# Kernel optimization log

Measured on AMD Instinct MI355X. Metric: run time of the kernel, lower is better.

The kernel has to match this reference:

```python
import jax, jax.numpy as jnp
import numpy as np

B, S, D, H, F = 2, 2048, 1024, 16, 4096
HD = D // H
EPS = 1e-5
NEG = -1e9


def _layernorm(x, g, b):
    mu = jnp.mean(x, axis=-1, keepdims=True)
    var = jnp.mean((x - mu) ** 2, axis=-1, keepdims=True)
    return (x - mu) * jax.lax.rsqrt(var + EPS) * g + b


def _attention(x, wq, wk, wv, wo, bo):
    b, s, d = x.shape
    q = (x @ wq).reshape(b, s, H, HD).transpose(0, 2, 1, 3)  # [b,h,s,hd]
    k = (x @ wk).reshape(b, s, H, HD).transpose(0, 2, 1, 3)
    v = (x @ wv).reshape(b, s, H, HD).transpose(0, 2, 1, 3)
    scores = jnp.einsum('bhqd,bhkd->bhqk', q, k) / (HD ** 0.5)
    # Faithful to source bug: masked_fill(mask == 0, -1e9) where mask = triu(diag=1)
    # -> positions with k <= q (lower triangle incl. diagonal) are filled with -1e9.
    lower = jnp.tril(jnp.ones((s, s), dtype=bool))
    scores = jnp.where(lower, NEG, scores)
    w = jax.nn.softmax(scores, axis=-1)
    o = jnp.einsum('bhqk,bhkd->bhqd', w, v)
    o = o.transpose(0, 2, 1, 3).reshape(b, s, d)
    return o @ wo + bo


def _ffn(x, w1, b1, w2, b2):
    return jax.nn.gelu(x @ w1 + b1, approximate=False) @ w2 + b2


def setup_inputs() -> dict:
    key = jax.random.key(0)
    ks = jax.random.split(key, 10)
    s = 0.02
    return {
        'x': jax.random.normal(ks[0], (B, S, D), jnp.float32),
        'wq': jax.random.normal(ks[1], (D, D), jnp.float32) * s,
        'wk': jax.random.normal(ks[2], (D, D), jnp.float32) * s,
        'wv': jax.random.normal(ks[3], (D, D), jnp.float32) * s,
        'wo': jax.random.normal(ks[4], (D, D), jnp.float32) * s,
        'bo': jnp.zeros((D,), jnp.float32),
        'ln1_g': jnp.ones((D,), jnp.float32),
        'ln1_b': jnp.zeros((D,), jnp.float32),
        'ln2_g': jnp.ones((D,), jnp.float32),
        'ln2_b': jnp.zeros((D,), jnp.float32),
        'w1': jax.random.normal(ks[5], (D, F), jnp.float32) * s,
        'b1': jnp.zeros((F,), jnp.float32),
        'w2': jax.random.normal(ks[6], (F, D), jnp.float32) * s,
        'b2': jnp.zeros((D,), jnp.float32),
    }


def reference(x, wq, wk, wv, wo, bo, ln1_g, ln1_b, ln2_g, ln2_b, w1, b1, w2, b2):
    shortcut = x
    h = _layernorm(x, ln1_g, ln1_b)
    h = _attention(h, wq, wk, wv, wo, bo)  # dropout = identity (eval)
    h = h + shortcut
    shortcut = h
    h2 = _layernorm(h, ln2_g, ln2_b)
    h2 = _attention(h2, wq, wk, wv, wo, bo)  # same attn module reused, per source
    h2 = _ffn(h2, w1, b1, w2, b2)
    return h2 + shortcut
```

## Files before the change

### kernel.cpp

```cpp
#include <hip/hip_runtime.h>
#include <hip/hip_bf16.h>
#include <math.h>

#define Bz 2
#define Sz 2048
#define Dz 1024
#define Hz 16
#define HDz 64
#define Fz 4096
#define ROWS (Bz*Sz)
#define EPSf 1e-5f
#define NEGf -1e9f

typedef __attribute__((ext_vector_type(8))) short short8;
typedef __attribute__((ext_vector_type(4))) float floatx4;

__device__ __forceinline__ unsigned short f2bf(float f){
  __hip_bfloat16 h = __float2bfloat16(f);
  return *(unsigned short*)&h;
}
__device__ __forceinline__ float bf2f(unsigned short u){
  union { unsigned x; float f; } a; a.x = ((unsigned)u) << 16; return a.f;
}

__device__ __forceinline__ float fast_gelu(float x){
  float t  = fabsf(x) * 0.70710678118654752f;
  float kk = __builtin_amdgcn_rcpf(1.0f + 0.3275911f * t);
  float poly = ((((1.061405429f*kk - 1.453152027f)*kk + 1.421413741f)*kk
                 - 0.284496736f)*kk + 0.254829592f)*kk;
  float er = 1.0f - poly * __expf(-t*t);
  er = copysignf(er, x);
  return 0.5f * x * (1.0f + er);
}

__device__ __forceinline__ void gload16(const void* g, void* l){
  __builtin_amdgcn_global_load_lds(
      (const __attribute__((address_space(1))) unsigned int*)g,
      (__attribute__((address_space(3))) unsigned int*)l, 16, 0, 0);
}

__device__ __forceinline__ void bar(){
  asm volatile("" ::: "memory");
  __builtin_amdgcn_s_barrier();
  asm volatile("" ::: "memory");
}
#define WAITV6 asm volatile("s_waitcnt vmcnt(6)" ::: "memory")
#define WAITV0 asm volatile("s_waitcnt vmcnt(0)" ::: "memory")
#define WL0    asm volatile("s_waitcnt lgkmcnt(0)" ::: "memory")

__device__ __forceinline__ void xcd_remap(int& bmblk, int& bnblk){
  int gx = gridDim.x, gy = gridDim.y;
  int id = blockIdx.y * gx + blockIdx.x;
  int xcd = id & 7, local = id >> 3;
  bnblk = local % gx;
  bmblk = xcd * (gy >> 3) + local / gx;
}

__global__ __launch_bounds__(256)
void transpose_cast(const float* __restrict__ W, unsigned short* __restrict__ Wt,
                    int K, int N)
{
  __shared__ unsigned short Ts[32][33];
  int n0 = blockIdx.x*32, k0 = blockIdx.y*32;
  int r = threadIdx.x >> 3, c0 = (threadIdx.x & 7) * 4;
  float4 w4 = *(const float4*)(W + (size_t)(k0+r)*N + n0 + c0);
  Ts[r][c0+0] = f2bf(w4.x); Ts[r][c0+1] = f2bf(w4.y);
  Ts[r][c0+2] = f2bf(w4.z); Ts[r][c0+3] = f2bf(w4.w);
  __syncthreads();
  unsigned v0 = Ts[c0+0][r], v1 = Ts[c0+1][r], v2 = Ts[c0+2][r], v3 = Ts[c0+3][r];
  uint2 p; p.x = v0 | (v1<<16); p.y = v2 | (v3<<16);
  *(uint2*)(Wt + (size_t)(n0+r)*K + k0 + c0) = p;
}

__global__ __launch_bounds__(256)
void ln_kernel(const float* __restrict__ in, const float* __restrict__ gam,
               const float* __restrict__ bet, unsigned short* __restrict__ out)
{
  int row = blockIdx.x, t = threadIdx.x;
  size_t base = (size_t)row * Dz;
  int c0 = t * 4;
  float4 x4 = *(const float4*)(in + base + c0);
  float v[4] = {x4.x, x4.y, x4.z, x4.w};
  float s = v[0]+v[1]+v[2]+v[3];
  #pragma unroll
  for (int off=32; off>0; off>>=1) s += __shfl_down(s, off, 64);
  __shared__ float ws[4];
  int lane = t & 63, wid = t >> 6;
  if (lane == 0) ws[wid] = s;
  __syncthreads();
  float mu = (ws[0]+ws[1]+ws[2]+ws[3]) * (1.0f/Dz);
  __syncthreads();
  float d0=v[0]-mu, d1=v[1]-mu, d2=v[2]-mu, d3=v[3]-mu;
  float s2 = d0*d0+d1*d1+d2*d2+d3*d3;
  #pragma unroll
  for (int off=32; off>0; off>>=1) s2 += __shfl_down(s2, off, 64);
  if (lane == 0) ws[wid] = s2;
  __syncthreads();
  float var = (ws[0]+ws[1]+ws[2]+ws[3]) * (1.0f/Dz);
  float rstd = rsqrtf(var + EPSf);
  float4 g4 = *(const float4*)(gam + c0);
  float4 b4 = *(const float4*)(bet + c0);
  unsigned r0 = f2bf((v[0]-mu)*rstd*g4.x + b4.x);
  unsigned r1 = f2bf((v[1]-mu)*rstd*g4.y + b4.y);
  unsigned r2 = f2bf((v[2]-mu)*rstd*g4.z + b4.z);
  unsigned r3 = f2bf((v[3]-mu)*rstd*g4.w + b4.w);
  uint2 p; p.x = r0 | (r1<<16); p.y = r2 | (r3<<16);
  *(uint2*)(out + base + c0) = p;
}

#define STG_A(buf, half, k0) { \
  _Pragma("unroll") for (int c_=0;c_<2;c_++){ \
    int sg_ = c_*8 + wave; \
    int row0_ = ((sg_>>3)<<7) + ((sg_&7)<<3) + ((half)<<6); \
    gload16(pA[half][c_] + (k0), &As[buf][row0_*64]); } }

#define STG_B(buf, jh, k0) { \
  _Pragma("unroll") for (int c_=0;c_<2;c_++){ \
    int sg_ = c_*8 + wave; int rho0_ = sg_<<3; \
    gload16(pB[jh][c_] + (k0), &Bs[buf][jh][rho0_*64]); } }

#define READ_A4(dst, buf, ihalf) { \
  _Pragma("unroll") for (int ii_=0; ii_<4; ++ii_){ \
    int row_ = wm*128 + ((ihalf)*4+ii_)*16 + l15; \
    _Pragma("unroll") for (int ks_=0; ks_<2; ++ks_){ \
      int slot_ = (ks_*4+quad) ^ (l15&7); \
      dst[ii_][ks_] = *(const short8*)&As[buf][row_*64 + slot_*8]; } } }

#define READ_B2(dst, buf, jh) { \
  _Pragma("unroll") for (int jl_=0; jl_<2; ++jl_){ \
    int rho_ = wn*32 + jl_*16 + l15; \
    _Pragma("unroll") for (int ks_=0; ks_<2; ++ks_){ \
      int slot_ = (ks_*4+quad) ^ (l15&7); \
      dst[jl_][ks_] = *(const short8*)&Bs[buf][jh][rho_*64 + slot_*8]; } } }

#define MFMA_PH(IH, JH, AF, BF) { \
  __builtin_amdgcn_s_setprio(1); \
  _Pragma("unroll") for (int ii_=0; ii_<4; ++ii_){ \
    _Pragma("unroll") for (int jl_=0; jl_<2; ++jl_){ \
      floatx4 c_ = acc[(IH)*4+ii_][(JH)*2+jl_]; \
      c_ = __builtin_amdgcn_mfma_f32_16x16x32_bf16(AF[ii_][0], BF[jl_][0], c_, 0,0,0); \
      c_ = __builtin_amdgcn_mfma_f32_16x16x32_bf16(AF[ii_][1], BF[jl_][1], c_, 0,0,0); \
      acc[(IH)*4+ii_][(JH)*2+jl_] = c_; } } \
  __builtin_amdgcn_s_setprio(0); }

__global__ __launch_bounds__(512, 2)
void gemm256(const unsigned short* __restrict__ A,
             const unsigned short* __restrict__ Bt,
             const float* __restrict__ bias, const float* __restrict__ res,
             float* __restrict__ outf, unsigned short* __restrict__ outb,
             int M, int N, int K, int lda, int ldb, int act, int qkvmode)
{
  __shared__ unsigned short As[2][256*64];
  __shared__ unsigned short Bs[2][2][128*64];

  int t = threadIdx.x;
  int wave = t >> 6, lane = t & 63;
  int l15 = lane & 15, quad = lane >> 4;
  int wm = wave >> 2, wn = wave & 3;

  int nN = gridDim.x, nM = gridDim.y;
  int id = blockIdx.y * nN + blockIdx.x;
  int xcd = id & 7, local = id >> 3;
  int bnblk = local % nN;
  int bmblk = xcd * (nM >> 3) + local / nN;
  int bm = bmblk * 256, bn = bnblk * 256;

  if (gridDim.z > 1){
    A    += (size_t)blockIdx.z * K;
    Bt   += (size_t)blockIdx.z * K;
    outf += (size_t)blockIdx.z * ((size_t)M * N);
  }

  int lrow = lane >> 3;
  int lcol = ((lane & 7) ^ (lane >> 3)) * 8;

  const unsigned short* pA[2][2];
  const unsigned short* pB[2][2];
  #pragma unroll
  for (int half=0; half<2; half++)
    #pragma unroll
    for (int c=0;c<2;c++){
      int sg = c*8 + wave;
      int row0 = ((sg>>3)<<7) + ((sg&7)<<3) + (half<<6);
      pA[half][c] = A + (size_t)(bm + row0 + lrow)*lda + lcol;
    }
  #pragma unroll
  for (int jh=0; jh<2; jh++)
    #pragma unroll
    for (int c=0;c<2;c++){
      int sg = c*8 + wave;
      int rho0 = sg<<3;
      int gn = ((rho0>>5)<<6) + (jh<<5) + (rho0&31);
      pB[jh][c] = Bt + (size_t)(bn + gn + lrow)*ldb + lcol;
    }

  floatx4 acc[8][4];
  #pragma unroll
  for (int i=0;i<8;i++)
    #pragma unroll
    for (int j=0;j<4;j++) acc[i][j] = (floatx4){0.f,0.f,0.f,0.f};

  STG_A(0, 0, 0);  STG_A(0, 1, 0);
  STG_B(0, 0, 0);  STG_B(0, 1, 0);
  STG_A(1, 0, 64); STG_A(1, 1, 64);
  STG_B(1, 0, 64);
  WAITV6;
  bar();

  int NKT = K >> 6;
  int nIter = NKT >> 1;
  for (int it = 0; it < nIter; ++it){
    bool more = (it + 1 < nIter);
    int k0B  = (2*it+1) << 6;
    int k0A2 = (2*it+2) << 6;
    int k0B2 = (2*it+3) << 6;
    short8 aLo[4][2], aHi[4][2], bcur[2][2];

    READ_A4(aLo, 0, 0);
    READ_B2(bcur, 0, 0);
    STG_B(1, 1, k0B);
    bar(); WL0;
    MFMA_PH(0, 0, aLo, bcur);
    bar();

    READ_A4(aHi, 0, 1);
    READ_B2(bcur, 0, 0);
    if (more) STG_A(0, 0, k0A2);
    bar(); WL0;
    MFMA_PH(1, 0, aHi, bcur);
    bar();

    READ_B2(bcur, 0, 1);
    if (more) STG_A(0, 1, k0A2);
    bar(); WL0;
    MFMA_PH(0, 1, aLo, bcur);
    bar();

    if (more) { STG_B(0, 0, k0A2); WAITV6; }
    else      { WAITV0; }
    bar();
    MFMA_PH(1, 1, aHi, bcur);
    bar();

    READ_A4(aLo, 1, 0);
    READ_B2(bcur, 1, 0);
    if (more) STG_B(0, 1, k0A2);
    bar(); WL0;
    MFMA_PH(0, 0, aLo, bcur);
    bar();

    READ_A4(aHi, 1, 1);
    READ_B2(bcur, 1, 0);
    if (more) STG_A(1, 0, k0B2);
    bar(); WL0;
    MFMA_PH(1, 0, aHi, bcur);
    bar();

    READ_B2(bcur, 1, 1);
    if (more) STG_A(1, 1, k0B2);
    bar(); WL0;
    MFMA_PH(0, 1, aLo, bcur);
    bar();

    if (more) { STG_B(1, 0, k0B2); WAITV6; }
    bar();
    MFMA_PH(1, 1, aHi, bcur);
    bar();
  }

  float bj[4];
  #pragma unroll
  for (int j=0;j<4;j++) bj[j] = bias ? bias[bn + wn*64 + j*16 + l15] : 0.f;

  size_t selbase = 0; int ncol = N; int bnl = bn;
  if (qkvmode){ selbase = (size_t)(bn >> 10) * ((size_t)M * 1024); ncol = 1024; bnl = bn & 1023; }

  #pragma unroll
  for (int i=0;i<8;i++){
    int row0 = bm + wm*128 + i*16 + quad*4;
    #pragma unroll
    for (int r=0;r<4;r++){
      size_t rowoff = selbase + (size_t)(row0 + r) * ncol;
      #pragma unroll
      for (int j=0;j<4;j++){
        float v = acc[i][j][r] + bj[j];
        if (act) v = fast_gelu(v);
        size_t off = rowoff + bnl + wn*64 + j*16 + l15;
        if (res) v += res[off];
        if (outf) outf[off] = v;
        else      outb[off] = f2bf(v);
      }
    }
  }
}

__global__ __launch_bounds__(256)
void gemm_n64(const unsigned short* __restrict__ A,
              const unsigned short* __restrict__ Bt,
              const float* __restrict__ bias, const float* __restrict__ res,
              float* __restrict__ outf, unsigned short* __restrict__ outb,
              int M, int N, int K)
{
  __shared__ unsigned short As[2][128*64];
  __shared__ unsigned short Bs[2][64*64];
  int t = threadIdx.x;
  int bmblk, bnblk; xcd_remap(bmblk, bnblk);
  int bm = bmblk * 128, bn = bnblk * 64;
  int wave = t >> 6, lane = t & 63;
  int l15 = lane & 15, quad = lane >> 4;
  int arow = lane >> 3;
  int acbg = ((lane & 7) ^ arow) * 8;
  const unsigned short* gA = A  + (size_t)(bm + wave*32 + arow)*K + acbg;
  const unsigned short* gB = Bt + (size_t)(bn + wave*16 + arow)*K + acbg;

  floatx4 acc[2][4];
  #pragma unroll
  for (int i=0;i<2;i++)
    #pragma unroll
    for (int j=0;j<4;j++) acc[i][j] = (floatx4){0.f,0.f,0.f,0.f};

  int swr = (l15 & 7);

  {
    unsigned short* lA = &As[0][wave*32*64];
    unsigned short* lB = &Bs[0][wave*16*64];
    gload16(gA,                 lA);
    gload16(gA + (size_t)8*K,   lA + 8*64);
    gload16(gA + (size_t)16*K,  lA + 16*64);
    gload16(gA + (size_t)24*K,  lA + 24*64);
    gload16(gB,                 lB);
    gload16(gB + (size_t)8*K,   lB + 8*64);
  }

  int nIter = K >> 6;
  for (int it = 0; it < nIter; ++it) {
    __syncthreads();
    int cur = it & 1;
    if (it + 1 < nIter) {
      int k1 = (it+1) << 6;
      unsigned short* lA = &As[cur^1][wave*32*64];
      unsigned short* lB = &Bs[cur^1][wave*16*64];
      gload16(gA + k1,                 lA);
      gload16(gA + k1 + (size_t)8*K,   lA + 8*64);
      gload16(gA + k1 + (size_t)16*K,  lA + 16*64);
      gload16(gA + k1 + (size_t)24*K,  lA + 24*64);
      gload16(gB + k1,                 lB);
      gload16(gB + k1 + (size_t)8*K,   lB + 8*64);
    }
    const unsigned short* Ac = As[cur];
    const unsigned short* Bc = Bs[cur];
    #pragma unroll
    for (int ks=0; ks<2; ++ks){
      short8 af[2], bf[4];
      #pragma unroll
      for (int i=0;i<2;i++)
        af[i] = *(const short8*)&Ac[(wave*32 + i*16 + l15)*64 + ((ks*4 + quad) ^ swr)*8];
      #pragma unroll
      for (int j=0;j<4;j++)
        bf[j] = *(const short8*)&Bc[(j*16 + l15)*64 + ((ks*4 + quad) ^ swr)*8];
      #pragma unroll
      for (int i=0;i<2;i++)
        #pragma unroll
        for (int j=0;j<4;j++)
          acc[i][j] = __builtin_amdgcn_mfma_f32_16x16x32_bf16(af[i], bf[j], acc[i][j], 0, 0, 0);
    }
  }

  float bj[4];
  #pragma unroll
  for (int j=0;j<4;j++) bj[j] = bias ? bias[bn + j*16 + l15] : 0.f;

  #pragma unroll
  for (int i=0;i<2;i++){
    int row0 = bm + wave*32 + i*16 + quad*4;
    #pragma unroll
    for (int r=0;r<4;r++){
      size_t rowoff = (size_t)(row0 + r) * N;
      #pragma unroll
      for (int j=0;j<4;j++){
        float v = acc[i][j][r] + bj[j];
        size_t off = rowoff + bn + j*16 + l15;
        if (res) v += res[off];
        if (outf) outf[off] = v;
        else      outb[off] = f2bf(v);
      }
    }
  }
}

__global__ __launch_bounds__(256)
void reduce4(const float* __restrict__ part, const float* __restrict__ bias,
             const float* __restrict__ res, float* __restrict__ out)
{
  const size_t NN = (size_t)ROWS * Dz;
  size_t i = ((size_t)blockIdx.x * 256 + threadIdx.x) * 4;
  float4 a = *(const float4*)(part + i);
  float4 b = *(const float4*)(part + NN + i);
  float4 c = *(const float4*)(part + 2*NN + i);
  float4 d = *(const float4*)(part + 3*NN + i);
  float4 r = *(const float4*)(res + i);
  int col = threadIdx.x * 4;
  float4 g = *(const float4*)(bias + col);
  float4 o;
  o.x = a.x+b.x+c.x+d.x + g.x + r.x;
  o.y = a.y+b.y+c.y+d.y + g.y + r.y;
  o.z = a.z+b.z+c.z+d.z + g.z + r.z;
  o.w = a.w+b.w+c.w+d.w + g.w + r.w;
  *(float4*)(out + i) = o;
}

__global__ __launch_bounds__(256)
void vmean_kernel(const unsigned short* __restrict__ v, float* __restrict__ vm)
{
  int h = blockIdx.x, b = blockIdx.y;
  int t = threadIdx.x, d = t & 63, seg = t >> 6;
  float s = 0.f;
  for (int i=0;i<512;i++){
    int srow = seg*512 + i;
    s += bf2f(v[((size_t)(b*Sz + srow))*Dz + h*HDz + d]);
  }
  __shared__ float red[4][64];
  red[seg][d] = s;
  __syncthreads();
  if (seg == 0){
    float tot = red[0][d]+red[1][d]+red[2][d]+red[3][d];
    vm[(b*Hz + h)*HDz + d] = tot * (1.0f/2048.0f);
  }
}

__global__ __launch_bounds__(256)
void attn_mfma(const unsigned short* __restrict__ Qg,
               const unsigned short* __restrict__ Kg,
               const unsigned short* __restrict__ Vg,
               const float* __restrict__ vmean,
               unsigned short* __restrict__ Og)
{
  __shared__ unsigned short Ks[128][72];
  __shared__ unsigned short Vts[64][136];
  __shared__ unsigned short Ps[128][72];

  int t = threadIdx.x;
  int wave = t >> 6, lane = t & 63;
  int l15 = lane & 15, quad = lane >> 4;
  int b = blockIdx.z, h = blockIdx.y;
  int qt = b ? (15 - (int)blockIdx.x) : (int)blockIdx.x;

  {
    int r = t >> 1, c = (t & 1) * 32;
    const unsigned short* qp = Qg + ((size_t)(b*Sz + qt*128 + r))*Dz + h*HDz + c;
    uint4 q0 = *(const uint4*)(qp);
    uint4 q1 = *(const uint4*)(qp + 8);
    uint4 q2 = *(const uint4*)(qp + 16);
    uint4 q3 = *(const uint4*)(qp + 24);
    *(uint4*)&Ps[r][c]      = q0;
    *(uint4*)&Ps[r][c + 8]  = q1;
    *(uint4*)&Ps[r][c + 16] = q2;
    *(uint4*)&Ps[r][c + 24] = q3;
  }
  __syncthreads();
  short8 aq[2][2];
  #pragma unroll
  for (int i=0;i<2;i++)
    #pragma unroll
    for (int ks=0;ks<2;ks++)
      aq[i][ks] = *(const short8*)&Ps[wave*32 + i*16 + l15][ks*32 + quad*8];

  floatx4 acc_o[2][4];
  #pragma unroll
  for (int i=0;i<2;i++)
    #pragma unroll
    for (int j=0;j<4;j++) acc_o[i][j] = (floatx4){0.f,0.f,0.f,0.f};
  float lacc[2][4];
  #pragma unroll
  for (int i=0;i<2;i++)
    #pragma unroll
    for (int r=0;r<4;r++) lacc[i][r] = 0.f;

  int sr = t >> 2, sc = (t & 3) * 16;

  uint4 pk0,pk1,pk2,pk3,pv0,pv1,pv2,pv3;
  {
    size_t off0 = ((size_t)(b*Sz + qt*128 + sr))*Dz + h*HDz + sc;
    size_t off1 = off0 + (size_t)64*Dz;
    pk0 = *(const uint4*)(Kg + off0); pk1 = *(const uint4*)(Kg + off0 + 8);
    pk2 = *(const uint4*)(Kg + off1); pk3 = *(const uint4*)(Kg + off1 + 8);
    pv0 = *(const uint4*)(Vg + off0); pv1 = *(const uint4*)(Vg + off0 + 8);
    pv2 = *(const uint4*)(Vg + off1); pv3 = *(const uint4*)(Vg + off1 + 8);
  }

  for (int jt2 = qt; jt2 < Sz/128; ++jt2) {
    __syncthreads();
    {
      *(uint4*)&Ks[sr][sc]        = pk0; *(uint4*)&Ks[sr][sc + 8]      = pk1;
      *(uint4*)&Ks[64 + sr][sc]   = pk2; *(uint4*)&Ks[64 + sr][sc + 8] = pk3;
      unsigned short e[16];
      e[0]=pv0.x&0xffff; e[1]=pv0.x>>16; e[2]=pv0.y&0xffff; e[3]=pv0.y>>16;
      e[4]=pv0.z&0xffff; e[5]=pv0.z>>16; e[6]=pv0.w&0xffff; e[7]=pv0.w>>16;
      e[8]=pv1.x&0xffff; e[9]=pv1.x>>16; e[10]=pv1.y&0xffff; e[11]=pv1.y>>16;
      e[12]=pv1.z&0xffff; e[13]=pv1.z>>16; e[14]=pv1.w&0xffff; e[15]=pv1.w>>16;
      #pragma unroll
      for (int j=0;j<16;j++) Vts[sc + j][sr] = e[j];
      e[0]=pv2.x&0xffff; e[1]=pv2.x>>16; e[2]=pv2.y&0xffff; e[3]=pv2.y>>16;
      e[4]=pv2.z&0xffff; e[5]=pv2.z>>16; e[6]=pv2.w&0xffff; e[7]=pv2.w>>16;
      e[8]=pv3.x&0xffff; e[9]=pv3.x>>16; e[10]=pv3.y&0xffff; e[11]=pv3.y>>16;
      e[12]=pv3.z&0xffff; e[13]=pv3.z>>16; e[14]=pv3.w&0xffff; e[15]=pv3.w>>16;
      #pragma unroll
      for (int j=0;j<16;j++) Vts[sc + j][64 + sr] = e[j];
    }
    __syncthreads();

    if (jt2 + 1 < Sz/128) {
      size_t off0 = ((size_t)(b*Sz + (jt2+1)*128 + sr))*Dz + h*HDz + sc;
      size_t off1 = off0 + (size_t)64*Dz;
      pk0 = *(const uint4*)(Kg + off0); pk1 = *(const uint4*)(Kg + off0 + 8);
      pk2 = *(const uint4*)(Kg + off1); pk3 = *(const uint4*)(Kg + off1 + 8);
      pv0 = *(const uint4*)(Vg + off0); pv1 = *(const uint4*)(Vg + off0 + 8);
      pv2 = *(const uint4*)(Vg + off1); pv3 = *(const uint4*)(Vg + off1 + 8);
    }

    #pragma unroll
    for (int hh=0; hh<2; ++hh){
      floatx4 acc_s[2][4];
      #pragma unroll
      for (int i=0;i<2;i++)
        #pragma unroll
        for (int j=0;j<4;j++) acc_s[i][j] = (floatx4){0.f,0.f,0.f,0.f};
      #pragma unroll
      for (int ks=0;ks<2;ks++){
        short8 bk[4];
        #pragma unroll
        for (int j=0;j<4;j++) bk[j] = *(const short8*)&Ks[hh*64 + j*16 + l15][ks*32 + quad*8];
        #pragma unroll
        for (int i=0;i<2;i++)
          #pragma unroll
          for (int j=0;j<4;j++)
            acc_s[i][j] = __builtin_amdgcn_mfma_f32_16x16x32_bf16(aq[i][ks], bk[j], acc_s[i][j], 0, 0, 0);
      }
      #pragma unroll
      for (int i=0;i<2;i++){
        #pragma unroll
        for (int j=0;j<4;j++){
          int kj = jt2*128 + hh*64 + j*16 + l15;
          #pragma unroll
          for (int r=0;r<4;r++){
            int qrow = qt*128 + wave*32 + i*16 + quad*4 + r;
            float s = acc_s[i][j][r] * 0.125f;
            if (kj <= qrow) s = NEGf;
            float p = __expf(fminf(s, 80.f));
            lacc[i][r] += p;
            Ps[wave*32 + i*16 + quad*4 + r][j*16 + l15] = f2bf(p);
          }
        }
      }
      #pragma unroll
      for (int ks=0;ks<2;ks++){
        short8 ap[2], bv[4];
        #pragma unroll
        for (int i=0;i<2;i++) ap[i] = *(const short8*)&Ps[wave*32 + i*16 + l15][ks*32 + quad*8];
        #pragma unroll
        for (int j=0;j<4;j++) bv[j] = *(const short8*)&Vts[j*16 + l15][hh*64 + ks*32 + quad*8];
        #pragma unroll
        for (int i=0;i<2;i++)
          #pragma unroll
          for (int j=0;j<4;j++)
            acc_o[i][j] = __builtin_amdgcn_mfma_f32_16x16x32_bf16(ap[i], bv[j], acc_o[i][j], 0, 0, 0);
      }
    }
  }

  #pragma unroll
  for (int i=0;i<2;i++){
    #pragma unroll
    for (int r=0;r<4;r++){
      float l = lacc[i][r];
      l += __shfl_xor(l, 1, 64);
      l += __shfl_xor(l, 2, 64);
      l += __shfl_xor(l, 4, 64);
      l += __shfl_xor(l, 8, 64);
      int qrow = qt*128 + wave*32 + i*16 + quad*4 + r;
      float inv = 1.0f / l;
      size_t rowoff = ((size_t)(b*Sz + qrow))*Dz + h*HDz;
      #pragma unroll
      for (int j=0;j<4;j++){
        float ov = acc_o[i][j][r] * inv;
        if (qrow == Sz-1) ov = vmean[(b*Hz + h)*HDz + j*16 + l15];
        Og[rowoff + j*16 + l15] = f2bf(ov);
      }
    }
  }
}

extern "C" void kernel_launch(void* const* d_in, const int* in_sizes, int n_in,
                              void* d_out, int out_size, void* d_ws, size_t ws_size,
                              hipStream_t stream)
{
  const float* x    = (const float*)d_in[0];
  const float* wq   = (const float*)d_in[1];
  const float* wk   = (const float*)d_in[2];
  const float* wv   = (const float*)d_in[3];
  const float* wo   = (const float*)d_in[4];
  const float* bo   = (const float*)d_in[5];
  const float* ln1g = (const float*)d_in[6];
  const float* ln1b = (const float*)d_in[7];
  const float* ln2g = (const float*)d_in[8];
  const float* ln2b = (const float*)d_in[9];
  const float* w1   = (const float*)d_in[10];
  const float* b1   = (const float*)d_in[11];
  const float* w2   = (const float*)d_in[12];
  const float* b2   = (const float*)d_in[13];
  float* out = (float*)d_out;

  const size_t MB = 1024*1024;
  char* w = (char*)d_ws;
  float*          trunk = (float*)(w);
  unsigned short* lnb   = (unsigned short*)(w + 16*MB);
  float*          vmean = (float*)(w + 16*MB);
  unsigned short* q     = (unsigned short*)(w + 24*MB);
  unsigned short* k     = (unsigned short*)(w + 32*MB);
  unsigned short* v     = (unsigned short*)(w + 40*MB);
  unsigned short* ctx   = (unsigned short*)(w + 48*MB);
  unsigned short* wqkvT = (unsigned short*)(w + 56*MB);
  unsigned short* wqT   = wqkvT;
  unsigned short* wkT   = (unsigned short*)(w + 58*MB);
  unsigned short* wvT   = (unsigned short*)(w + 60*MB);
  unsigned short* woT   = (unsigned short*)(w + 62*MB);
  unsigned short* w1T   = (unsigned short*)(w + 64*MB);
  unsigned short* w2T   = (unsigned short*)(w + 72*MB);
  unsigned short* mid   = (unsigned short*)(w + 24*MB);
  float*          part  = (float*)(w + 80*MB);
  bool splitk = ws_size >= (size_t)144*MB;

  dim3 blk(256), blk512(512);
  transpose_cast<<<dim3(32,32),  blk, 0, stream>>>(wq, wqT, Dz, Dz);
  transpose_cast<<<dim3(32,32),  blk, 0, stream>>>(wk, wkT, Dz, Dz);
  transpose_cast<<<dim3(32,32),  blk, 0, stream>>>(wv, wvT, Dz, Dz);
  transpose_cast<<<dim3(32,32),  blk, 0, stream>>>(wo, woT, Dz, Dz);
  transpose_cast<<<dim3(128,32), blk, 0, stream>>>(w1, w1T, Dz, Fz);
  transpose_cast<<<dim3(32,128), blk, 0, stream>>>(w2, w2T, Fz, Dz);

  dim3 gln(ROWS);
  dim3 gqkv(3*Dz/256, ROWS/256);
  dim3 gf1(Fz/256,  ROWS/256);
  dim3 gn64(Dz/64,  ROWS/128);
  dim3 gattn(Sz/128, Hz, Bz);
  dim3 gvm(Hz, Bz);

  ln_kernel<<<gln, blk, 0, stream>>>(x, ln1g, ln1b, lnb);
  gemm256<<<gqkv, blk512, 0, stream>>>(lnb, wqkvT, nullptr, nullptr, nullptr, q, ROWS, 3*Dz, Dz, Dz, Dz, 0, 1);
  vmean_kernel<<<gvm, blk, 0, stream>>>(v, vmean);
  attn_mfma<<<gattn, blk, 0, stream>>>(q, k, v, vmean, ctx);
  gemm_n64<<<gn64, blk, 0, stream>>>(ctx, woT, bo, x, trunk, nullptr, ROWS, Dz, Dz);

  ln_kernel<<<gln, blk, 0, stream>>>(trunk, ln2g, ln2b, lnb);
  gemm256<<<gqkv, blk512, 0, stream>>>(lnb, wqkvT, nullptr, nullptr, nullptr, q, ROWS, 3*Dz, Dz, Dz, Dz, 0, 1);
  vmean_kernel<<<gvm, blk, 0, stream>>>(v, vmean);
  attn_mfma<<<gattn, blk, 0, stream>>>(q, k, v, vmean, ctx);
  gemm_n64<<<gn64, blk, 0, stream>>>(ctx, woT, bo, nullptr, nullptr, lnb, ROWS, Dz, Dz);
  gemm256<<<gf1, blk512, 0, stream>>>(lnb, w1T, b1, nullptr, nullptr, mid, ROWS, Fz, Dz, Dz, Dz, 1, 0);
  if (splitk) {
    gemm256<<<dim3(4,16,4), blk512, 0, stream>>>(mid, w2T, nullptr, nullptr, part, nullptr, ROWS, Dz, Fz/4, Fz, Fz, 0, 0);
    reduce4<<<dim3(4096), blk, 0, stream>>>(part, b2, trunk, out);
  } else {
    gemm_n64<<<gn64, blk, 0, stream>>>(mid, w2T, b2, trunk, out, nullptr, ROWS, Dz, Fz);
  }
}
```

Baseline: 540.1 us.

## Pre-transpose V globally and use XOR-swizzled LDS layouts for K and V in attention

Adds a bf16 transpose kernel that writes V as [b,h,d,s] into scratch space borrowed from the output buffer. The attention kernel can then load V^T tiles with vector stores instead of scattering 16 scalar LDS writes per thread. K and V^T tiles now use unpadded LDS layouts with XOR swizzling to avoid bank conflicts. The cost is an extra transpose launch and its memory traffic per attention call, plus reliance on the output buffer being free as scratch until the final kernel writes it.

```diff
diff --git a/kernel.cpp b/kernel.cpp
--- a/kernel.cpp
+++ b/kernel.cpp
@@ -70,6 +70,25 @@
   unsigned v0 = Ts[c0+0][r], v1 = Ts[c0+1][r], v2 = Ts[c0+2][r], v3 = Ts[c0+3][r];
   uint2 p; p.x = v0 | (v1<<16); p.y = v2 | (v3<<16);
   *(uint2*)(Wt + (size_t)(n0+r)*K + k0 + c0) = p;
+}
+
+__global__ __launch_bounds__(256)
+void transpose_bf(const unsigned short* __restrict__ V, unsigned short* __restrict__ VT)
+{
+  __shared__ unsigned short Ts[32][33];
+  int st = blockIdx.x*32;
+  int R0 = blockIdx.y*32;
+  int b = R0 >> 10, hd0 = R0 & 1023;
+  int r = threadIdx.x >> 3, c0 = (threadIdx.x & 7) * 4;
+  uint2 w = *(const uint2*)(V + (size_t)(b*Sz + st + r)*Dz + hd0 + c0);
+  Ts[r][c0+0] = (unsigned short)(w.x & 0xffff);
+  Ts[r][c0+1] = (unsigned short)(w.x >> 16);
+  Ts[r][c0+2] = (unsigned short)(w.y & 0xffff);
+  Ts[r][c0+3] = (unsigned short)(w.y >> 16);
+  __syncthreads();
+  unsigned v0 = Ts[c0+0][r], v1 = Ts[c0+1][r], v2 = Ts[c0+2][r], v3 = Ts[c0+3][r];
+  uint2 p; p.x = v0 | (v1<<16); p.y = v2 | (v3<<16);
+  *(uint2*)(VT + (size_t)(R0+r)*Sz + st + c0) = p;
 }
 
 __global__ __launch_bounds__(256)
@@ -431,12 +450,12 @@
 __global__ __launch_bounds__(256)
 void attn_mfma(const unsigned short* __restrict__ Qg,
                const unsigned short* __restrict__ Kg,
-               const unsigned short* __restrict__ Vg,
+               const unsigned short* __restrict__ VTg,
                const float* __restrict__ vmean,
                unsigned short* __restrict__ Og)
 {
-  __shared__ unsigned short Ks[128][72];
-  __shared__ unsigned short Vts[64][136];
+  __shared__ unsigned short Ks[128*64];
+  __shared__ unsigned short Vts[64*128];
   __shared__ unsigned short Ps[128][72];
 
   int t = threadIdx.x;
@@ -477,6 +496,9 @@
     for (int r=0;r<4;r++) lacc[i][r] = 0.f;
 
   int sr = t >> 2, sc = (t & 3) * 16;
+  int kc2 = (t & 3) * 2, ksw = sr & 7;
+  int vd = t >> 2, vc = t & 3, vsw = vd & 7;
+  const unsigned short* vrow = VTg + ((size_t)((b*Hz + h)*64 + vd))*Sz;
 
   uint4 pk0,pk1,pk2,pk3,pv0,pv1,pv2,pv3;
   {
@@ -484,28 +506,23 @@
     size_t off1 = off0 + (size_t)64*Dz;
     pk0 = *(const uint4*)(Kg + off0); pk1 = *(const uint4*)(Kg + off0 + 8);
     pk2 = *(const uint4*)(Kg + off1); pk3 = *(const uint4*)(Kg + off1 + 8);
-    pv0 = *(const uint4*)(Vg + off0); pv1 = *(const uint4*)(Vg + off0 + 8);
-    pv2 = *(const uint4*)(Vg + off1); pv3 = *(const uint4*)(Vg + off1 + 8);
+    int vo = qt*128 + vc*32;
+    pv0 = *(const uint4*)(vrow + vo);      pv1 = *(const uint4*)(vrow + vo + 8);
+    pv2 = *(const uint4*)(vrow + vo + 16); pv3 = *(const uint4*)(vrow + vo + 24);
   }
 
   for (int jt2 = qt; jt2 < Sz/128; ++jt2) {
     __syncthreads();
     {
-      *(uint4*)&Ks[sr][sc]        = pk0; *(uint4*)&Ks[sr][sc + 8]      = pk1;
-      *(uint4*)&Ks[64 + sr][sc]   = pk2; *(uint4*)&Ks[64 + sr][sc + 8] = pk3;
-      unsigned short e[16];
-      e[0]=pv0.x&0xffff; e[1]=pv0.x>>16; e[2]=pv0.y&0xffff; e[3]=pv0.y>>16;
-      e[4]=pv0.z&0xffff; e[5]=pv0.z>>16; e[6]=pv0.w&0xffff; e[7]=pv0.w>>16;
-      e[8]=pv1.x&0xffff; e[9]=pv1.x>>16; e[10]=pv1.y&0xffff; e[11]=pv1.y>>16;
-      e[12]=pv1.z&0xffff; e[13]=pv1.z>>16; e[14]=pv1.w&0xffff; e[15]=pv1.w>>16;
-      #pragma unroll
-      for (int j=0;j<16;j++) Vts[sc + j][sr] = e[j];
-      e[0]=pv2.x&0xffff; e[1]=pv2.x>>16; e[2]=pv2.y&0xffff; e[3]=pv2.y>>16;
-      e[4]=pv2.z&0xffff; e[5]=pv2.z>>16; e[6]=pv2.w&0xffff; e[7]=pv2.w>>16;
-      e[8]=pv3.x&0xffff; e[9]=pv3.x>>16; e[10]=pv3.y&0xffff; e[11]=pv3.y>>16;
-      e[12]=pv3.z&0xffff; e[13]=pv3.z>>16; e[14]=pv3.w&0xffff; e[15]=pv3.w>>16;
-      #pragma unroll
-      for (int j=0;j<16;j++) Vts[sc + j][64 + sr] = e[j];
+      *(uint4*)&Ks[sr*64      + ((kc2  ) ^ ksw)*8] = pk0;
+      *(uint4*)&Ks[sr*64      + ((kc2+1) ^ ksw)*8] = pk1;
+      *(uint4*)&Ks[(64+sr)*64 + ((kc2  ) ^ ksw)*8] = pk2;
+      *(uint4*)&Ks[(64+sr)*64 + ((kc2+1) ^ ksw)*8] = pk3;
+      int k80 = vc*4;
+      *(uint4*)&Vts[vd*128 + (((k80+0)&8) | (((k80+0)^vsw)&7))*8] = pv0;
+      *(uint4*)&Vts[vd*128 + (((k80+1)&8) | (((k80+1)^vsw)&7))*8] = pv1;
+      *(uint4*)&Vts[vd*128 + (((k80+2)&8) | (((k80+2)^vsw)&7))*8] = pv2;
+      *(uint4*)&Vts[vd*128 + (((k80+3)&8) | (((k80+3)^vsw)&7))*8] = pv3;
     }
     __syncthreads();
 
@@ -514,8 +531,9 @@
       size_t off1 = off0 + (size_t)64*Dz;
       pk0 = *(const uint4*)(Kg + off0); pk1 = *(const uint4*)(Kg + off0 + 8);
       pk2 = *(const uint4*)(Kg + off1); pk3 = *(const uint4*)(Kg + off1 + 8);
-      pv0 = *(const uint4*)(Vg + off0); pv1 = *(const uint4*)(Vg + off0 + 8);
-      pv2 = *(const uint4*)(Vg + off1); pv3 = *(const uint4*)(Vg + off1 + 8);
+      int vo = (jt2+1)*128 + vc*32;
+      pv0 = *(const uint4*)(vrow + vo);      pv1 = *(const uint4*)(vrow + vo + 8);
+      pv2 = *(const uint4*)(vrow + vo + 16); pv3 = *(const uint4*)(vrow + vo + 24);
     }
 
     #pragma unroll
@@ -529,7 +547,8 @@
       for (int ks=0;ks<2;ks++){
         short8 bk[4];
         #pragma unroll
-        for (int j=0;j<4;j++) bk[j] = *(const short8*)&Ks[hh*64 + j*16 + l15][ks*32 + quad*8];
+        for (int j=0;j<4;j++)
+          bk[j] = *(const short8*)&Ks[(hh*64 + j*16 + l15)*64 + (((ks*4+quad) ^ (l15&7)))*8];
         #pragma unroll
         for (int i=0;i<2;i++)
           #pragma unroll
@@ -558,7 +577,8 @@
         #pragma unroll
         for (int i=0;i<2;i++) ap[i] = *(const short8*)&Ps[wave*32 + i*16 + l15][ks*32 + quad*8];
         #pragma unroll
-        for (int j=0;j<4;j++) bv[j] = *(const short8*)&Vts[j*16 + l15][hh*64 + ks*32 + quad*8];
+        for (int j=0;j<4;j++)
+          bv[j] = *(const short8*)&Vts[(j*16 + l15)*128 + (hh*8 + ((ks*4+quad) ^ (l15&7)))*8];
         #pragma unroll
         for (int i=0;i<2;i++)
           #pragma unroll
@@ -614,7 +634,6 @@
   char* w = (char*)d_ws;
   float*          trunk = (float*)(w);
   unsigned short* lnb   = (unsigned short*)(w + 16*MB);
-  float*          vmean = (float*)(w + 16*MB);
   unsigned short* q     = (unsigned short*)(w + 24*MB);
   unsigned short* k     = (unsigned short*)(w + 32*MB);
   unsigned short* v     = (unsigned short*)(w + 40*MB);
@@ -630,6 +649,9 @@
   float*          part  = (float*)(w + 80*MB);
   bool splitk = ws_size >= (size_t)144*MB;
 
+  unsigned short* vT    = (unsigned short*)d_out;
+  float*          vmean = (float*)((char*)d_out + 8*MB);
+
   dim3 blk(256), blk512(512);
   transpose_cast<<<dim3(32,32),  blk, 0, stream>>>(wq, wqT, Dz, Dz);
   transpose_cast<<<dim3(32,32),  blk, 0, stream>>>(wk, wkT, Dz, Dz);
@@ -644,17 +666,20 @@
   dim3 gn64(Dz/64,  ROWS/128);
   dim3 gattn(Sz/128, Hz, Bz);
   dim3 gvm(Hz, Bz);
+  dim3 gvt(Sz/32, Bz*Hz*HDz/32);
 
   ln_kernel<<<gln, blk, 0, stream>>>(x, ln1g, ln1b, lnb);
   gemm256<<<gqkv, blk512, 0, stream>>>(lnb, wqkvT, nullptr, nullptr, nullptr, q, ROWS, 3*Dz, Dz, Dz, Dz, 0, 1);
+  transpose_bf<<<gvt, blk, 0, stream>>>(v, vT);
   vmean_kernel<<<gvm, blk, 0, stream>>>(v, vmean);
-  attn_mfma<<<gattn, blk, 0, stream>>>(q, k, v, vmean, ctx);
+  attn_mfma<<<gattn, blk, 0, stream>>>(q, k, vT, vmean, ctx);
   gemm_n64<<<gn64, blk, 0, stream>>>(ctx, woT, bo, x, trunk, nullptr, ROWS, Dz, Dz);
 
   ln_kernel<<<gln, blk, 0, stream>>>(trunk, ln2g, ln2b, lnb);
   gemm256<<<gqkv, blk512, 0, stream>>>(lnb, wqkvT, nullptr, nullptr, nullptr, q, ROWS, 3*Dz, Dz, Dz, Dz, 0, 1);
+  transpose_bf<<<gvt, blk, 0, stream>>>(v, vT);
   vmean_kernel<<<gvm, blk, 0, stream>>>(v, vmean);
-  attn_mfma<<<gattn, blk, 0, stream>>>(q, k, v, vmean, ctx);
+  attn_mfma<<<gattn, blk, 0, stream>>>(q, k, vT, vmean, ctx);
   gemm_n64<<<gn64, blk, 0, stream>>>(ctx, woT, bo, nullptr, nullptr, lnb, ROWS, Dz, Dz);
   gemm256<<<gf1, blk512, 0, stream>>>(lnb, w1T, b1, nullptr, nullptr, mid, ROWS, Fz, Dz, Dz, Dz, 1, 0);
   if (splitk) {
```

After: 537.5 us. About the same (-0.5%).
